# Kernel tuning notes

Measured on AMD Instinct MI355X. Metric: run time of the kernel, lower is better.

## Reference

```python
import jax, jax.numpy as jnp
import numpy as np
import math

D_MODEL = 512
N_HEADS = 8
HEAD_DIM = D_MODEL // N_HEADS


def setup_inputs() -> dict:
    key = jax.random.key(0)
    k1, k2, k3 = jax.random.split(key, 3)
    B, T = 2, 4096
    x = jax.random.normal(k1, (B, T, D_MODEL), dtype=jnp.float32)
    # nn.Linear weights: stored as [out, in], applied as x @ W.T
    W_QKV = jax.random.normal(k2, (3 * D_MODEL, D_MODEL), dtype=jnp.float32) * (1.0 / math.sqrt(D_MODEL))
    W_O = jax.random.normal(k3, (D_MODEL, D_MODEL), dtype=jnp.float32) * (1.0 / math.sqrt(D_MODEL))
    return {"x": x, "W_QKV": W_QKV, "W_O": W_O}


def reference(x, W_QKV, W_O):
    B, T, C = x.shape
    qkv = (x @ W_QKV.T).reshape(B, T, 3, N_HEADS, HEAD_DIM)
    q, k, v = qkv[:, :, 0], qkv[:, :, 1], qkv[:, :, 2]  # [B,T,H,D]
    # scores: [B,H,T,T]
    scale = math.sqrt(HEAD_DIM)
    attn = jnp.einsum('bqhd,bkhd->bhqk', q, k) / scale
    causal_mask = jnp.triu(jnp.ones((T, T), dtype=bool), k=1)
    attn = jnp.where(causal_mask, -jnp.inf, attn)
    attn = jax.nn.softmax(attn, axis=-1)
    out = jnp.einsum('bhqk,bkhd->bqhd', attn, v).reshape(B, T, C)
    return out @ W_O.T
```

## Files before the change

kernel.cpp:

```cpp
#include <hip/hip_runtime.h>
#include <hip/hip_bf16.h>

typedef __bf16 bf16_t;
typedef __bf16 bf16x8 __attribute__((ext_vector_type(8)));
typedef __bf16 bf16x4 __attribute__((ext_vector_type(4)));
typedef float  floatx4 __attribute__((ext_vector_type(4)));

static __device__ __forceinline__ floatx4 mfma16(bf16x8 a, bf16x8 b, floatx4 c) {
  return __builtin_amdgcn_mfma_f32_16x16x32_bf16(a, b, c, 0, 0, 0);
}

typedef __attribute__((address_space(3))) void lds_vp;
typedef __attribute__((address_space(1))) void glb_vp;
#define GLDS16(g, l) \
  __builtin_amdgcn_global_load_lds((glb_vp*)(g), (lds_vp*)(l), 16, 0, 0)

__global__ void cvt_all_kernel(const float* __restrict__ x,
                               const float* __restrict__ wqkv,
                               const float* __restrict__ wo,
                               bf16_t* __restrict__ xb,
                               bf16_t* __restrict__ wqkvb,
                               bf16_t* __restrict__ wob) {
  int i = blockIdx.x * blockDim.x + threadIdx.x;
  const float4* src; bf16x4* dst; int off;
  if (i < 1048576)      { src = (const float4*)x;    dst = (bf16x4*)xb;    off = i; }
  else if (i < 1245184) { src = (const float4*)wqkv; dst = (bf16x4*)wqkvb; off = i - 1048576; }
  else                  { src = (const float4*)wo;   dst = (bf16x4*)wob;   off = i - 1245184; }
  float4 v = src[off];
  bf16x4 o;
  o[0] = (bf16_t)v.x; o[1] = (bf16_t)v.y; o[2] = (bf16_t)v.z; o[3] = (bf16_t)v.w;
  dst[off] = o;
}

__global__ __launch_bounds__(256) void gemm_qkv(
    const bf16_t* __restrict__ A, const bf16_t* __restrict__ B,
    bf16_t* __restrict__ Qo, bf16_t* __restrict__ Ko, bf16_t* __restrict__ Vto)
{
  __shared__ __align__(16) bf16_t As[2][128 * 64];
  __shared__ __align__(16) bf16_t Bs[2][128 * 64];
  const int tid  = threadIdx.x;
  const int lane = tid & 63;
  const int w    = tid >> 6;
  const int quad = lane >> 4;
  const int l15  = lane & 15;
  const int l7   = lane & 7;
  const int wm   = w & 1;
  const int wn   = w >> 1;
  const int K    = 512;

  floatx4 acc[4][4];
  #pragma unroll
  for (int i = 0; i < 4; ++i)
    #pragma unroll
    for (int j = 0; j < 4; ++j)
      acc[i][j] = (floatx4){0.f, 0.f, 0.f, 0.f};

  const bf16_t* Ab = A + (size_t)blockIdx.x * 128 * K;
  const bf16_t* Bb = B + (size_t)blockIdx.y * 128 * K;

  auto stage = [&](int buf, int k0) {
    #pragma unroll
    for (int i = 0; i < 4; ++i) {
      int c = tid + 256 * i;
      int row = c >> 3, colc = c & 7;
      int gofs = ((colc ^ (row & 7)) << 3);
      GLDS16(&Ab[(size_t)row * K + k0 + gofs], &As[buf][c * 8]);
      GLDS16(&Bb[(size_t)row * K + k0 + gofs], &Bs[buf][c * 8]);
    }
  };

  stage(0, 0);
  for (int it = 0; it < 8; ++it) {
    const int cur = it & 1;
    __syncthreads();
    if (it + 1 < 8) stage(cur ^ 1, (it + 1) << 6);
    #pragma unroll
    for (int ks = 0; ks < 2; ++ks) {
      bf16x8 af[4], bfr[4];
      #pragma unroll
      for (int t = 0; t < 4; ++t) {
        af[t]  = *(const bf16x8*)&As[cur][(wm * 64 + t * 16 + l15) * 64 +
                                         (((ks * 4 + quad) ^ l7) << 3)];
        bfr[t] = *(const bf16x8*)&Bs[cur][(wn * 64 + t * 16 + l15) * 64 +
                                         (((ks * 4 + quad) ^ l7) << 3)];
      }
      #pragma unroll
      for (int mt = 0; mt < 4; ++mt)
        #pragma unroll
        for (int nt = 0; nt < 4; ++nt)
          acc[mt][nt] = mfma16(af[mt], bfr[nt], acc[mt][nt]);
    }
  }

  if (blockIdx.y < 8) {
    #pragma unroll
    for (int mt = 0; mt < 4; ++mt) {
      #pragma unroll
      for (int nt = 0; nt < 4; ++nt) {
        #pragma unroll
        for (int r = 0; r < 4; ++r) {
          int m = blockIdx.x * 128 + wm * 64 + mt * 16 + quad * 4 + r;
          int n = blockIdx.y * 128 + wn * 64 + nt * 16 + l15;
          float v = acc[mt][nt][r];
          int b = m >> 12, t = m & 4095;
          int h = (n >> 6) & 7, d = n & 63;
          size_t bh = (size_t)(b * 8 + h);
          if (n < 512)
            Qo[bh * 262144 + (size_t)t * 64 + d] = (bf16_t)(v * 0.18033688f);
          else
            Ko[bh * 262144 + (size_t)t * 64 + d] = (bf16_t)v;
        }
      }
    }
  } else {
    __syncthreads();
    bf16_t* L = &As[0][0];
    #pragma unroll
    for (int mt = 0; mt < 4; ++mt)
      #pragma unroll
      for (int nt = 0; nt < 4; ++nt) {
        int n_l = wn * 64 + nt * 16 + l15;
        int mc  = wm * 8 + mt * 2 + (quad >> 1);
        bf16x4 v4;
        #pragma unroll
        for (int r = 0; r < 4; ++r) v4[r] = (bf16_t)acc[mt][nt][r];
        *(bf16x4*)&L[n_l * 128 + ((mc ^ (n_l & 15)) << 3) + (quad & 1) * 4] = v4;
      }
    __syncthreads();
    const int t0 = (blockIdx.x & 31) * 128;
    const int b  = blockIdx.x >> 5;
    #pragma unroll
    for (int i = 0; i < 8; ++i) {
      int c = tid + 256 * i;
      int n_l = c >> 4, tc = c & 15;
      int h = ((blockIdx.y - 8) << 1) | (n_l >> 6);
      int d = n_l & 63;
      size_t bh = (size_t)(b * 8 + h);
      int base0 = (tc >> 2) * 32 + (tc & 3) * 4;
      bf16x4 lo = *(const bf16x4*)&L[n_l * 128 +
                     (((base0 >> 3) ^ (n_l & 15)) << 3) + (base0 & 7)];
      bf16x4 hi = *(const bf16x4*)&L[n_l * 128 +
                     ((((base0 + 16) >> 3) ^ (n_l & 15)) << 3) + (base0 & 7)];
      bf16x8 o;
      #pragma unroll
      for (int e = 0; e < 4; ++e) { o[e] = lo[e]; o[e + 4] = hi[e]; }
      *(bf16x8*)&Vto[bh * 262144 + (size_t)d * 4096 + t0 + tc * 8] = o;
    }
  }
}

__global__ __launch_bounds__(256) void gemm_out(
    const bf16_t* __restrict__ A, const bf16_t* __restrict__ B,
    float* __restrict__ Cf)
{
  __shared__ __align__(16) bf16_t As[2][64 * 64];
  __shared__ __align__(16) bf16_t Bs[2][128 * 64];
  const int tid  = threadIdx.x;
  const int lane = tid & 63;
  const int w    = tid >> 6;
  const int quad = lane >> 4;
  const int l15  = lane & 15;
  const int l7   = lane & 7;

  floatx4 acc[4][2];
  #pragma unroll
  for (int i = 0; i < 4; ++i)
    #pragma unroll
    for (int j = 0; j < 2; ++j)
      acc[i][j] = (floatx4){0.f, 0.f, 0.f, 0.f};

  const bf16_t* Ab = A + (size_t)blockIdx.x * 64 * 512;
  const bf16_t* Bb = B + (size_t)blockIdx.y * 128 * 512;

  auto stage = [&](int buf, int k0) {
    #pragma unroll
    for (int i = 0; i < 2; ++i) {
      int c = tid + 256 * i;
      int row = c >> 3, colc = c & 7;
      GLDS16(&Ab[(size_t)row * 512 + k0 + ((colc ^ (row & 7)) << 3)],
             &As[buf][c * 8]);
    }
    #pragma unroll
    for (int i = 0; i < 4; ++i) {
      int c = tid + 256 * i;
      int row = c >> 3, colc = c & 7;
      GLDS16(&Bb[(size_t)row * 512 + k0 + ((colc ^ (row & 7)) << 3)],
             &Bs[buf][c * 8]);
    }
  };

  stage(0, 0);
  for (int it = 0; it < 8; ++it) {
    const int cur = it & 1;
    __syncthreads();
    if (it + 1 < 8) stage(cur ^ 1, (it + 1) << 6);
    #pragma unroll
    for (int ks = 0; ks < 2; ++ks) {
      bf16x8 af[4], bfr[2];
      #pragma unroll
      for (int t = 0; t < 4; ++t)
        af[t]  = *(const bf16x8*)&As[cur][(t * 16 + l15) * 64 +
                                         (((ks * 4 + quad) ^ l7) << 3)];
      #pragma unroll
      for (int t = 0; t < 2; ++t)
        bfr[t] = *(const bf16x8*)&Bs[cur][(w * 32 + t * 16 + l15) * 64 +
                                         (((ks * 4 + quad) ^ l7) << 3)];
      #pragma unroll
      for (int mt = 0; mt < 4; ++mt)
        #pragma unroll
        for (int nt = 0; nt < 2; ++nt)
          acc[mt][nt] = mfma16(af[mt], bfr[nt], acc[mt][nt]);
    }
  }

  #pragma unroll
  for (int mt = 0; mt < 4; ++mt)
    #pragma unroll
    for (int nt = 0; nt < 2; ++nt)
      #pragma unroll
      for (int r = 0; r < 4; ++r) {
        int m = blockIdx.x * 64 + mt * 16 + quad * 4 + r;
        int n = blockIdx.y * 128 + w * 32 + nt * 16 + l15;
        Cf[(size_t)m * 512 + n] = acc[mt][nt][r];
      }
}

__global__ __launch_bounds__(512, 4) void attn_kernel(
    const bf16_t* __restrict__ Qg, const bf16_t* __restrict__ Kgl,
    const bf16_t* __restrict__ Vtg, bf16_t* __restrict__ Og)
{
  __shared__ __align__(16) bf16_t Ks[2][128 * 64];
  __shared__ __align__(16) bf16_t Vts[2][64 * 128];

  const int tid  = threadIdx.x;
  const int lane = tid & 63;
  const int w    = tid >> 6;
  const int grp  = w >> 2;
  const int ws   = w & 3;
  const int quad = lane >> 4;
  const int l15  = lane & 15;

  const int id = blockIdx.x + 32 * blockIdx.y;
  const int k8 = id & 7;
  const int j  = id >> 3;
  const int jj = j & 31;
  const int bh = 2 * k8 + (jj & 1);
  const int p  = jj >> 1;
  const int x    = (j < 32) ? p : 15 - p;
  const int half = (j < 32) ? 0 : 1;
  const int qtA = 31 - x, qtB = x;
  const int qt_g = grp ? qtB : qtA;
  const size_t bh_off = (size_t)bh * 262144;
  const int b = bh >> 3, h = bh & 7;

  const int gq = qt_g * 128 + half * 64 + ws * 16 + l15;
  bf16x8 aq0, aq1;
  {
    const bf16_t* Qp = Qg + bh_off + (size_t)gq * 64;
    aq0 = *(const bf16x8*)&Qp[quad * 8];
    aq1 = *(const bf16x8*)&Qp[32 + quad * 8];
  }
  bf16x8 ones;
  #pragma unroll
  for (int i = 0; i < 8; ++i) ones[i] = (bf16_t)1.0f;

  floatx4 acc_o[4], acc_l;
  #pragma unroll
  for (int dt = 0; dt < 4; ++dt) acc_o[dt] = (floatx4){0.f, 0.f, 0.f, 0.f};
  acc_l = (floatx4){0.f, 0.f, 0.f, 0.f};

  auto stage = [&](int buf, int kt) {
    const bf16_t* Kp = Kgl + bh_off + (size_t)kt * 8192;
    const bf16_t* Vp = Vtg + bh_off + (size_t)kt * 128;
    #pragma unroll
    for (int i = 0; i < 2; ++i) {
      int c = tid + 512 * i;
      int row = c >> 3, colc = c & 7;
      GLDS16(&Kp[row * 64 + ((colc ^ (row & 7)) << 3)], &Ks[buf][c * 8]);
    }
    #pragma unroll
    for (int i = 0; i < 2; ++i) {
      int c = tid + 512 * i;
      int row = c >> 4, colc = c & 15;
      GLDS16(&Vp[(size_t)row * 4096 + ((colc ^ (row & 15)) << 3)], &Vts[buf][c * 8]);
    }
  };

  stage(0, 0);
  const int nkt = qtA + 1;
  for (int kt = 0; kt < nkt; ++kt) {
    const int cur = kt & 1;
    __syncthreads();
    if (kt + 1 < nkt) stage(cur ^ 1, kt + 1);

    if (kt <= qt_g) {
      floatx4 s[8];
      #pragma unroll
      for (int nt = 0; nt < 8; ++nt) s[nt] = (floatx4){0.f, 0.f, 0.f, 0.f};
      #pragma unroll
      for (int nt = 0; nt < 8; ++nt) {
        bf16x8 bk0 = *(const bf16x8*)&Ks[cur][(nt * 16 + l15) * 64 +
                                             ((quad ^ (l15 & 7)) << 3)];
        s[nt] = mfma16(bk0, aq0, s[nt]);
      }
      #pragma unroll
      for (int nt = 0; nt < 8; ++nt) {
        bf16x8 bk1 = *(const bf16x8*)&Ks[cur][(nt * 16 + l15) * 64 +
                                             (((4 + quad) ^ (l15 & 7)) << 3)];
        s[nt] = mfma16(bk1, aq1, s[nt]);
      }

      if (kt == qt_g) {
        #pragma unroll
        for (int nt = 0; nt < 8; ++nt)
          #pragma unroll
          for (int r = 0; r < 4; ++r)
            if (kt * 128 + nt * 16 + quad * 4 + r > gq) s[nt][r] = -3.0e38f;
      }
      #pragma unroll
      for (int nt = 0; nt < 8; ++nt)
        #pragma unroll
        for (int r = 0; r < 4; ++r)
          s[nt][r] = exp2f(s[nt][r]);

      #pragma unroll
      for (int kc = 0; kc < 4; ++kc) {
        bf16x8 pb;
        #pragma unroll
        for (int r = 0; r < 4; ++r) {
          pb[r]     = (bf16_t)s[kc * 2][r];
          pb[r + 4] = (bf16_t)s[kc * 2 + 1][r];
        }
        acc_l = mfma16(ones, pb, acc_l);
        #pragma unroll
        for (int dt = 0; dt < 4; ++dt) {
          int row = dt * 16 + l15;
          bf16x8 av = *(const bf16x8*)&Vts[cur][row * 128 +
                                               (((kc * 4 + quad) ^ l15) << 3)];
          acc_o[dt] = mfma16(av, pb, acc_o[dt]);
        }
      }
    }
  }

  __syncthreads();
  bf16_t* Ot = &Ks[0][grp * 4096];
  const float rl = 1.0f / acc_l[0];
  const int t_own = ws * 16 + l15;
  #pragma unroll
  for (int dt = 0; dt < 4; ++dt) {
    bf16x4 o4;
    #pragma unroll
    for (int r = 0; r < 4; ++r) o4[r] = (bf16_t)(acc_o[dt][r] * rl);
    *(bf16x4*)&Ot[t_own * 64 +
                  (((dt * 2 + (quad >> 1)) ^ (t_own & 7)) << 3) + (quad & 1) * 4] = o4;
  }
  __syncthreads();
  const int gtid = tid & 255;
  #pragma unroll
  for (int i = 0; i < 2; ++i) {
    int cc = gtid + 256 * i;
    int t = cc >> 3, c = cc & 7;
    bf16x8 o8 = *(const bf16x8*)&Ot[t * 64 + ((c ^ (t & 7)) << 3)];
    int trow = qt_g * 128 + half * 64 + t;
    *(bf16x8*)&Og[((size_t)b * 4096 + trow) * 512 + h * 64 + c * 8] = o8;
  }
}

extern "C" void kernel_launch(void* const* d_in, const int* in_sizes, int n_in,
                              void* d_out, int out_size, void* d_ws, size_t ws_size,
                              hipStream_t stream) {
  const float* x    = (const float*)d_in[0];
  const float* wqkv = (const float*)d_in[1];
  const float* wo   = (const float*)d_in[2];
  float* out = (float*)d_out;

  char* ws = (char*)d_ws;
  bf16_t* xb    = (bf16_t*)(ws);
  bf16_t* wqkvb = (bf16_t*)(ws + 8388608);
  bf16_t* wob   = (bf16_t*)(ws + 9961472);
  bf16_t* Qb    = (bf16_t*)(ws + 10485760);
  bf16_t* Kb    = (bf16_t*)(ws + 18874368);
  bf16_t* Vtb   = (bf16_t*)(ws + 27262976);
  bf16_t* Ob    = xb;

  cvt_all_kernel<<<5120, 256, 0, stream>>>(x, wqkv, wo, xb, wqkvb, wob);

  gemm_qkv<<<dim3(64, 12), 256, 0, stream>>>(xb, wqkvb, Qb, Kb, Vtb);
  attn_kernel<<<dim3(32, 16), 512, 0, stream>>>(Qb, Kb, Vtb, Ob);
  gemm_out<<<dim3(128, 4), 256, 0, stream>>>(Ob, wob, out);
}
```

Baseline: 164.4 us.

## Have each attention wave process two query blocks to reuse K/V fragments

Each wave in the attention kernel now handles 32 query rows (two 16-row blocks) instead of 16. This lets every K and V LDS fragment read feed two MFMAs, and it halves the grid to 256 blocks that each cover a full 128-row tile pair. The change also swaps exp2f for the raw hardware exp2 builtin and relaxes launch bounds to 2 blocks per CU. The cost is higher register pressure and fewer blocks, and therefore less parallelism across the CUs.

```diff
diff --git a/kernel.cpp b/kernel.cpp
--- a/kernel.cpp
+++ b/kernel.cpp
@@ -225,7 +225,7 @@
       }
 }
 
-__global__ __launch_bounds__(512, 4) void attn_kernel(
+__global__ __launch_bounds__(512, 2) void attn_kernel(
     const bf16_t* __restrict__ Qg, const bf16_t* __restrict__ Kgl,
     const bf16_t* __restrict__ Vtg, bf16_t* __restrict__ Og)
 {
@@ -235,39 +235,42 @@
   const int tid  = threadIdx.x;
   const int lane = tid & 63;
   const int w    = tid >> 6;
-  const int grp  = w >> 2;
-  const int ws   = w & 3;
+  const int grp2 = w >> 1;
+  const int tileB = grp2 >> 1;
+  const int half  = grp2 & 1;
+  const int ws2   = w & 1;
   const int quad = lane >> 4;
   const int l15  = lane & 15;
 
-  const int id = blockIdx.x + 32 * blockIdx.y;
+  const int id = blockIdx.x;
   const int k8 = id & 7;
   const int j  = id >> 3;
-  const int jj = j & 31;
-  const int bh = 2 * k8 + (jj & 1);
-  const int p  = jj >> 1;
-  const int x    = (j < 32) ? p : 15 - p;
-  const int half = (j < 32) ? 0 : 1;
+  const int bh = 2 * k8 + (j & 1);
+  const int x  = j >> 1;
   const int qtA = 31 - x, qtB = x;
-  const int qt_g = grp ? qtB : qtA;
+  const int qt_g = tileB ? qtB : qtA;
   const size_t bh_off = (size_t)bh * 262144;
   const int b = bh >> 3, h = bh & 7;
 
-  const int gq = qt_g * 128 + half * 64 + ws * 16 + l15;
-  bf16x8 aq0, aq1;
-  {
-    const bf16_t* Qp = Qg + bh_off + (size_t)gq * 64;
-    aq0 = *(const bf16x8*)&Qp[quad * 8];
-    aq1 = *(const bf16x8*)&Qp[32 + quad * 8];
+  const int gq0 = qt_g * 128 + half * 64 + ws2 * 32 + l15;
+  bf16x8 aqk0[2], aqk1[2];
+  #pragma unroll
+  for (int qb = 0; qb < 2; ++qb) {
+    const bf16_t* Qp = Qg + bh_off + (size_t)(gq0 + qb * 16) * 64;
+    aqk0[qb] = *(const bf16x8*)&Qp[quad * 8];
+    aqk1[qb] = *(const bf16x8*)&Qp[32 + quad * 8];
   }
   bf16x8 ones;
   #pragma unroll
   for (int i = 0; i < 8; ++i) ones[i] = (bf16_t)1.0f;
 
-  floatx4 acc_o[4], acc_l;
-  #pragma unroll
-  for (int dt = 0; dt < 4; ++dt) acc_o[dt] = (floatx4){0.f, 0.f, 0.f, 0.f};
-  acc_l = (floatx4){0.f, 0.f, 0.f, 0.f};
+  floatx4 acc_o[2][4], acc_l[2];
+  #pragma unroll
+  for (int qb = 0; qb < 2; ++qb) {
+    #pragma unroll
+    for (int dt = 0; dt < 4; ++dt) acc_o[qb][dt] = (floatx4){0.f, 0.f, 0.f, 0.f};
+    acc_l[qb] = (floatx4){0.f, 0.f, 0.f, 0.f};
+  }
 
   auto stage = [&](int buf, int kt) {
     const bf16_t* Kp = Kgl + bh_off + (size_t)kt * 8192;
@@ -288,78 +291,91 @@
 
   stage(0, 0);
   const int nkt = qtA + 1;
+  const floatx4 z4 = (floatx4){0.f, 0.f, 0.f, 0.f};
   for (int kt = 0; kt < nkt; ++kt) {
     const int cur = kt & 1;
     __syncthreads();
     if (kt + 1 < nkt) stage(cur ^ 1, kt + 1);
 
     if (kt <= qt_g) {
-      floatx4 s[8];
-      #pragma unroll
-      for (int nt = 0; nt < 8; ++nt) s[nt] = (floatx4){0.f, 0.f, 0.f, 0.f};
+      floatx4 s[2][8];
       #pragma unroll
       for (int nt = 0; nt < 8; ++nt) {
         bf16x8 bk0 = *(const bf16x8*)&Ks[cur][(nt * 16 + l15) * 64 +
                                              ((quad ^ (l15 & 7)) << 3)];
-        s[nt] = mfma16(bk0, aq0, s[nt]);
+        s[0][nt] = mfma16(bk0, aqk0[0], z4);
+        s[1][nt] = mfma16(bk0, aqk0[1], z4);
       }
       #pragma unroll
       for (int nt = 0; nt < 8; ++nt) {
         bf16x8 bk1 = *(const bf16x8*)&Ks[cur][(nt * 16 + l15) * 64 +
                                              (((4 + quad) ^ (l15 & 7)) << 3)];
-        s[nt] = mfma16(bk1, aq1, s[nt]);
+        s[0][nt] = mfma16(bk1, aqk1[0], s[0][nt]);
+        s[1][nt] = mfma16(bk1, aqk1[1], s[1][nt]);
       }
 
       if (kt == qt_g) {
+        #pragma unroll
+        for (int qb = 0; qb < 2; ++qb)
+          #pragma unroll
+          for (int nt = 0; nt < 8; ++nt)
+            #pragma unroll
+            for (int r = 0; r < 4; ++r)
+              if (kt * 128 + nt * 16 + quad * 4 + r > gq0 + qb * 16)
+                s[qb][nt][r] = -3.0e38f;
+      }
+      #pragma unroll
+      for (int qb = 0; qb < 2; ++qb)
         #pragma unroll
         for (int nt = 0; nt < 8; ++nt)
           #pragma unroll
           for (int r = 0; r < 4; ++r)
-            if (kt * 128 + nt * 16 + quad * 4 + r > gq) s[nt][r] = -3.0e38f;
-      }
-      #pragma unroll
-      for (int nt = 0; nt < 8; ++nt)
-        #pragma unroll
-        for (int r = 0; r < 4; ++r)
-          s[nt][r] = exp2f(s[nt][r]);
+            s[qb][nt][r] = __builtin_amdgcn_exp2f(s[qb][nt][r]);
 
       #pragma unroll
       for (int kc = 0; kc < 4; ++kc) {
-        bf16x8 pb;
-        #pragma unroll
-        for (int r = 0; r < 4; ++r) {
-          pb[r]     = (bf16_t)s[kc * 2][r];
-          pb[r + 4] = (bf16_t)s[kc * 2 + 1][r];
-        }
-        acc_l = mfma16(ones, pb, acc_l);
+        bf16x8 pb[2];
+        #pragma unroll
+        for (int qb = 0; qb < 2; ++qb)
+          #pragma unroll
+          for (int r = 0; r < 4; ++r) {
+            pb[qb][r]     = (bf16_t)s[qb][kc * 2][r];
+            pb[qb][r + 4] = (bf16_t)s[qb][kc * 2 + 1][r];
+          }
+        acc_l[0] = mfma16(ones, pb[0], acc_l[0]);
+        acc_l[1] = mfma16(ones, pb[1], acc_l[1]);
         #pragma unroll
         for (int dt = 0; dt < 4; ++dt) {
           int row = dt * 16 + l15;
           bf16x8 av = *(const bf16x8*)&Vts[cur][row * 128 +
                                                (((kc * 4 + quad) ^ l15) << 3)];
-          acc_o[dt] = mfma16(av, pb, acc_o[dt]);
+          acc_o[0][dt] = mfma16(av, pb[0], acc_o[0][dt]);
+          acc_o[1][dt] = mfma16(av, pb[1], acc_o[1][dt]);
         }
       }
     }
   }
 
   __syncthreads();
-  bf16_t* Ot = &Ks[0][grp * 4096];
-  const float rl = 1.0f / acc_l[0];
-  const int t_own = ws * 16 + l15;
-  #pragma unroll
-  for (int dt = 0; dt < 4; ++dt) {
-    bf16x4 o4;
-    #pragma unroll
-    for (int r = 0; r < 4; ++r) o4[r] = (bf16_t)(acc_o[dt][r] * rl);
-    *(bf16x4*)&Ot[t_own * 64 +
-                  (((dt * 2 + (quad >> 1)) ^ (t_own & 7)) << 3) + (quad & 1) * 4] = o4;
+  bf16_t* Ot = &Ks[0][grp2 * 4096];
+  #pragma unroll
+  for (int qb = 0; qb < 2; ++qb) {
+    const float rl = 1.0f / acc_l[qb][0];
+    const int t_own = ws2 * 32 + qb * 16 + l15;
+    #pragma unroll
+    for (int dt = 0; dt < 4; ++dt) {
+      bf16x4 o4;
+      #pragma unroll
+      for (int r = 0; r < 4; ++r) o4[r] = (bf16_t)(acc_o[qb][dt][r] * rl);
+      *(bf16x4*)&Ot[t_own * 64 +
+                    (((dt * 2 + (quad >> 1)) ^ (t_own & 7)) << 3) + (quad & 1) * 4] = o4;
+    }
   }
   __syncthreads();
-  const int gtid = tid & 255;
-  #pragma unroll
-  for (int i = 0; i < 2; ++i) {
-    int cc = gtid + 256 * i;
+  const int gtid = tid & 127;
+  #pragma unroll
+  for (int i = 0; i < 4; ++i) {
+    int cc = gtid + 128 * i;
     int t = cc >> 3, c = cc & 7;
     bf16x8 o8 = *(const bf16x8*)&Ot[t * 64 + ((c ^ (t & 7)) << 3)];
     int trow = qt_g * 128 + half * 64 + t;
@@ -387,6 +403,6 @@
   cvt_all_kernel<<<5120, 256, 0, stream>>>(x, wqkv, wo, xb, wqkvb, wob);
 
   gemm_qkv<<<dim3(64, 12), 256, 0, stream>>>(xb, wqkvb, Qb, Kb, Vtb);
-  attn_kernel<<<dim3(32, 16), 512, 0, stream>>>(Qb, Kb, Vtb, Ob);
+  attn_kernel<<<dim3(256), 512, 0, stream>>>(Qb, Kb, Vtb, Ob);
   gemm_out<<<dim3(128, 4), 256, 0, stream>>>(Ob, wob, out);
 }
```

Result: faster. 153.0 us (-6.9%).
